# Performance work log

Hardware: AMD Instinct MI355X
Metric: run time of the kernel (lower is better)

## Reference

```python
import jax, jax.numpy as jnp
import numpy as np

B, N, E, D, R, T, L = 4, 20000, 320000, 64, 64, 1000, 6
LN_EPS = 1e-5


def setup_inputs() -> dict:
    key = jax.random.key(0)
    ks = jax.random.split(key, 20)
    inp = {
        "edge_index": jax.random.randint(ks[0], (2, E), 0, N),
        "edge_type": jax.random.randint(ks[1], (E,), 0, R),
        "relation_representations": jax.random.normal(ks[2], (B, R, D), jnp.float32),
        "h_index": jax.random.randint(ks[3], (B,), 0, N),
        "r_index": jax.random.randint(ks[4], (B,), 0, R),
        "t_index": jax.random.randint(ks[5], (B, T), 0, N),
        "edge_weight": jnp.ones((E,), jnp.float32),
        # per-layer relation-projection MLP (Linear,ReLU,Linear)
        "rp_w1": jax.random.normal(ks[6], (L, D, D), jnp.float32) / np.sqrt(D),
        "rp_b1": jnp.zeros((L, D), jnp.float32),
        "rp_w2": jax.random.normal(ks[7], (L, D, D), jnp.float32) / np.sqrt(D),
        "rp_b2": jnp.zeros((L, D), jnp.float32),
        # per-layer update linear: concat([input, aggregated]) -> D
        "conv_w": jax.random.normal(ks[8], (L, 2 * D, D), jnp.float32) / np.sqrt(2 * D),
        "conv_b": jnp.zeros((L, D), jnp.float32),
        "ln_g": jnp.ones((L, D), jnp.float32),
        "ln_b": jnp.zeros((L, D), jnp.float32),
        # final MLP (num_mlp_layers=2): feature_dim = D (last hidden) + D (query) = 2D
        "mlp_w1": jax.random.normal(ks[9], (2 * D, 2 * D), jnp.float32) / np.sqrt(2 * D),
        "mlp_b1": jnp.zeros((2 * D,), jnp.float32),
        "mlp_w2": jax.random.normal(ks[10], (2 * D, 1), jnp.float32) / np.sqrt(2 * D),
        "mlp_b2": jnp.zeros((1,), jnp.float32),
    }
    return inp


def reference(edge_index, edge_type, relation_representations, h_index, r_index,
              t_index, edge_weight, rp_w1, rp_b1, rp_w2, rp_b2, conv_w, conv_b,
              ln_g, ln_b, mlp_w1, mlp_b1, mlp_w2, mlp_b2):
    # --- boundary: scatter query embedding onto source node per query ---
    query = relation_representations[jnp.arange(B), r_index]              # [B, D]
    boundary = jnp.zeros((B, N, D), jnp.float32).at[jnp.arange(B), h_index].add(query)
    src, dst = edge_index[0], edge_index[1]

    def layer(x, params):
        w1, b1, w2, b2, cw, cb, g, b = params
        # project_relations MLP on query relation representations
        rel = jax.nn.relu(jnp.einsum('brd,de->bre', relation_representations, w1) + b1)
        rel = jnp.einsum('brd,de->bre', rel, w2) + b2                     # [B, R, D]
        # distmult message: h[src] * rel[edge_type], weighted
        msg = x[:, src, :] * rel[:, edge_type, :] * edge_weight[None, :, None]  # [B, E, D]
        agg = jax.ops.segment_sum(msg.transpose(1, 0, 2), dst,
                                  num_segments=N).transpose(1, 0, 2)
        agg = agg + boundary                                              # boundary self-loop
        h = jnp.concatenate([x, agg], axis=-1) @ cw + cb                  # [B, N, D]
        mu = h.mean(-1, keepdims=True)
        var = h.var(-1, keepdims=True)
        h = (h - mu) * jax.lax.rsqrt(var + LN_EPS) * g + b                # layer norm
        h = jax.nn.relu(h)
        return h + x, None                                                # short_cut

    x, _ = jax.lax.scan(layer, boundary,
                        (rp_w1, rp_b1, rp_w2, rp_b2, conv_w, conv_b, ln_g, ln_b))
    node_query = jnp.broadcast_to(query[:, None, :], (B, N, D))
    output = jnp.concatenate([x, node_query], axis=-1)                    # [B, N, 2D]
    feat = jnp.take_along_axis(output, t_index[:, :, None], axis=1)       # [B, T, 2D]
    h = jax.nn.relu(feat @ mlp_w1 + mlp_b1)
    score = (h @ mlp_w2 + mlp_b2).squeeze(-1)                             # [B, T]
    return score
```

## Files before the change

kernel.cpp:

```cpp
#include <hip/hip_runtime.h>
#include <hip/hip_fp16.h>

#define NB 4
#define NN 20000
#define NE 320000
#define ND 64
#define NR 64
#define NT 1000
#define NL 6
#define LN_EPS 1e-5f
#define CAP 64

typedef _Float16 half8 __attribute__((ext_vector_type(8)));
typedef _Float16 half4v __attribute__((ext_vector_type(4)));
typedef float floatx4 __attribute__((ext_vector_type(4)));


__global__ void __launch_bounds__(256)
prep1(int* __restrict__ cnt,
      const float* __restrict__ cw, _Float16* __restrict__ cwt,
      const float* __restrict__ relrep, const int* __restrict__ r_index,
      float* __restrict__ query,
      const float* __restrict__ rp_w1, const float* __restrict__ rp_b1,
      const float* __restrict__ rp_w2, const float* __restrict__ rp_b2,
      __half* __restrict__ rel16) {
    int blk = blockIdx.x, tid = threadIdx.x;
    if (blk < 79) {
        int i = blk * 256 + tid;
        if (i < NN) cnt[i] = 0;
    } else if (blk < 271) {
        int i = (blk - 79) * 256 + tid;
        int l = i >> 13, rem = i & 8191, k = rem >> 6, n = rem & 63;
        cwt[l * 8192 + n * 128 + k] = (_Float16)cw[i];
    } else if (blk == 271) {
        int b = tid >> 6, d = tid & 63;
        query[tid] = relrep[(b * NR + r_index[b]) * ND + d];
    } else {
        int u = blk - 272;
        int l = u >> 6, r = u & 63;
        int b = tid >> 6, j = tid & 63;
        const float* w1 = rp_w1 + l * ND * ND;
        const float* w2 = rp_w2 + l * ND * ND;
        float xin = relrep[(b * NR + r) * ND + j];
        float acc = rp_b1[l * ND + j];
        #pragma unroll 8
        for (int k = 0; k < ND; ++k) acc += __shfl(xin, k) * w1[k * ND + j];
        float hmid = fmaxf(acc, 0.f);
        float outv = rp_b2[l * ND + j];
        #pragma unroll 8
        for (int k = 0; k < ND; ++k) outv += __shfl(hmid, k) * w2[k * ND + j];
        rel16[l * (NR * NB * ND) + (r * NB + b) * ND + j] = __float2half(outv);
    }
}

__global__ void __launch_bounds__(256)
prep2(const int* __restrict__ ei, const int* __restrict__ et,
      const float* __restrict__ ew, int* __restrict__ cnt,
      int4* __restrict__ epack) {
    int e = blockIdx.x * 256 + threadIdx.x;
    int d = ei[NE + e];
    int p = atomicAdd(&cnt[d], 1);
    if (p < CAP)
        epack[d * CAP + p] = make_int4(ei[e], et[e], __float_as_int(ew[e]), 0);
}

__device__ __forceinline__ float2 h2f(unsigned u) {
    __half2 h = *(__half2*)&u;
    return __half22float2(h);
}
__device__ __forceinline__ __half2 u2h2(unsigned u) { return *(__half2*)&u; }

__device__ __forceinline__ void conv_ln_epilogue(
        _Float16* A16, float* sD, int wv, int lane, int n,
        const _Float16* __restrict__ cwt, const float* __restrict__ cb,
        const float* __restrict__ g, const float* __restrict__ bb,
        __half* __restrict__ xo16) {
    __syncthreads();
    {
        int m = lane & 15, quad = lane >> 4;
        int ncol = wv * 16 + m;
        floatx4 acc = {0.f, 0.f, 0.f, 0.f};
        #pragma unroll
        for (int k0 = 0; k0 < 128; k0 += 32) {
            half8 a = *(const half8*)&A16[m * 136 + k0 + quad * 8];
            half8 bfr = *(const half8*)&cwt[ncol * 128 + k0 + quad * 8];
            acc = __builtin_amdgcn_mfma_f32_16x16x32_f16(a, bfr, acc, 0, 0, 0);
        }
        #pragma unroll
        for (int rg = 0; rg < 4; ++rg)
            sD[(quad * 4 + rg) * 65 + ncol] = acc[rg];
    }
    __syncthreads();
    float gl = g[lane], bl = bb[lane], cbl = cb[lane];
    #pragma unroll
    for (int b = 0; b < NB; ++b) {
        float acc = sD[(wv * 4 + b) * 65 + lane] + cbl;
        float s = acc, s2 = acc * acc;
        #pragma unroll
        for (int o = 32; o > 0; o >>= 1) { s += __shfl_xor(s, o); s2 += __shfl_xor(s2, o); }
        float mu  = s * (1.f / ND);
        float var = s2 * (1.f / ND) - mu * mu;
        float hn  = (acc - mu) * rsqrtf(var + LN_EPS) * gl + bl;
        float xvf = (float)A16[(wv * 4 + b) * 136 + lane];
        float v   = fmaxf(hn, 0.f) + xvf;
        xo16[(n * NB + b) * ND + lane] = __float2half(v);
    }
}

__global__ void __launch_bounds__(256)
fused_layer_first(const __half* __restrict__ rel16,
                  const int* __restrict__ cnt, const int4* __restrict__ epack,
                  const float* __restrict__ query, const int* __restrict__ h_index,
                  const _Float16* __restrict__ cwt, const float* __restrict__ cb,
                  const float* __restrict__ g, const float* __restrict__ bb,
                  __half* __restrict__ xo16) {
    __shared__ _Float16 A16[16 * 136];
    __shared__ float sD[16 * 65];
    int wv = threadIdx.x >> 6;
    int lane = threadIdx.x & 63;
    int n = blockIdx.x * 4 + wv;
    int cn = min(cnt[n], CAP);
    int bidx = lane >> 4, c4 = (lane & 15) << 2;
    int hb = h_index[bidx];

    const uint2* __restrict__ r2 = (const uint2*)rel16;
    float4 q4 = ((const float4*)query)[lane];
    half4v qh;
    qh.x = (_Float16)q4.x; qh.y = (_Float16)q4.y;
    qh.z = (_Float16)q4.z; qh.w = (_Float16)q4.w;
    float qx = (float)qh.x, qy = (float)qh.y, qz = (float)qh.z, qw = (float)qh.w;

    float4 agg4 = make_float4(0.f, 0.f, 0.f, 0.f);
    {
        int4 ed = make_int4(0, 0, 0, 0);
        if (lane < cn) ed = epack[n * CAP + lane];
        for (int j = 0; j < cn; ++j) {
            int s   = __shfl(ed.x, j);
            int t   = __shfl(ed.y, j);
            float w = __int_as_float(__shfl(ed.z, j));
            if (s == hb) {
                uint2 ra = r2[t * 64 + lane];
                float2 q0 = h2f(ra.x), q1 = h2f(ra.y);
                agg4.x = fmaf(qx * q0.x, w, agg4.x);
                agg4.y = fmaf(qy * q0.y, w, agg4.y);
                agg4.z = fmaf(qz * q1.x, w, agg4.z);
                agg4.w = fmaf(qw * q1.y, w, agg4.w);
            }
        }
    }
    if (n == hb) {
        agg4.x += q4.x; agg4.y += q4.y; agg4.z += q4.z; agg4.w += q4.w;
    }
    {
        int r = wv * 4 + bidx;
        half4v xh = {0, 0, 0, 0};
        if (n == hb) xh = qh;
        *(half4v*)&A16[r * 136 + c4] = xh;
        half4v ah;
        ah.x = (_Float16)agg4.x; ah.y = (_Float16)agg4.y;
        ah.z = (_Float16)agg4.z; ah.w = (_Float16)agg4.w;
        *(half4v*)&A16[r * 136 + 64 + c4] = ah;
    }
    conv_ln_epilogue(A16, sD, wv, lane, n, cwt, cb, g, bb, xo16);
}

__global__ void __launch_bounds__(256)
fused_layer(const __half* __restrict__ x16, const __half* __restrict__ rel16,
            const int* __restrict__ cnt, const int4* __restrict__ epack,
            const float* __restrict__ query, const int* __restrict__ h_index,
            const _Float16* __restrict__ cwt, const float* __restrict__ cb,
            const float* __restrict__ g, const float* __restrict__ bb,
            __half* __restrict__ xo16) {
    __shared__ _Float16 A16[16 * 136];
    __shared__ float sD[16 * 65];
    int wv = threadIdx.x >> 6;
    int lane = threadIdx.x & 63;
    int n = blockIdx.x * 4 + wv;
    int cn = min(cnt[n], CAP);
    int hf = lane >> 5, sub = lane & 31;

    const uint4* __restrict__ x4 = (const uint4*)x16;
    const uint4* __restrict__ r4 = (const uint4*)rel16;

    float acc[8] = {0.f, 0.f, 0.f, 0.f, 0.f, 0.f, 0.f, 0.f};
    {
        int4 ed = make_int4(0, 0, 0, 0);
        if (lane < cn) ed = epack[n * CAP + lane];
        int j = 0;
        for (; j + 4 <= cn; j += 4) {
            int ja = j + hf, jb = j + 2 + hf;
            int sa = __shfl(ed.x, ja), ta = __shfl(ed.y, ja);
            int sb = __shfl(ed.x, jb), tb = __shfl(ed.y, jb);
            float wa = __int_as_float(__shfl(ed.z, ja));
            float wb = __int_as_float(__shfl(ed.z, jb));
            uint4 xa = x4[sa * 32 + sub], ra = r4[ta * 32 + sub];
            uint4 xb = x4[sb * 32 + sub], rb = r4[tb * 32 + sub];
            __half2 p0, p1, p2, p3;
            p0 = __hmul2(u2h2(xa.x), u2h2(ra.x));
            p1 = __hmul2(u2h2(xa.y), u2h2(ra.y));
            p2 = __hmul2(u2h2(xa.z), u2h2(ra.z));
            p3 = __hmul2(u2h2(xa.w), u2h2(ra.w));
            acc[0] = fmaf(__low2float(p0),  wa, acc[0]);
            acc[1] = fmaf(__high2float(p0), wa, acc[1]);
            acc[2] = fmaf(__low2float(p1),  wa, acc[2]);
            acc[3] = fmaf(__high2float(p1), wa, acc[3]);
            acc[4] = fmaf(__low2float(p2),  wa, acc[4]);
            acc[5] = fmaf(__high2float(p2), wa, acc[5]);
            acc[6] = fmaf(__low2float(p3),  wa, acc[6]);
            acc[7] = fmaf(__high2float(p3), wa, acc[7]);
            p0 = __hmul2(u2h2(xb.x), u2h2(rb.x));
            p1 = __hmul2(u2h2(xb.y), u2h2(rb.y));
            p2 = __hmul2(u2h2(xb.z), u2h2(rb.z));
            p3 = __hmul2(u2h2(xb.w), u2h2(rb.w));
            acc[0] = fmaf(__low2float(p0),  wb, acc[0]);
            acc[1] = fmaf(__high2float(p0), wb, acc[1]);
            acc[2] = fmaf(__low2float(p1),  wb, acc[2]);
            acc[3] = fmaf(__high2float(p1), wb, acc[3]);
            acc[4] = fmaf(__low2float(p2),  wb, acc[4]);
            acc[5] = fmaf(__high2float(p2), wb, acc[5]);
            acc[6] = fmaf(__low2float(p3),  wb, acc[6]);
            acc[7] = fmaf(__high2float(p3), wb, acc[7]);
        }
        for (; j < cn; j += 2) {
            int ja = j + hf;
            int sa = __shfl(ed.x, ja), ta = __shfl(ed.y, ja);
            float wa = __int_as_float(__shfl(ed.z, ja));
            uint4 xa = x4[sa * 32 + sub], ra = r4[ta * 32 + sub];
            __half2 p0 = __hmul2(u2h2(xa.x), u2h2(ra.x));
            __half2 p1 = __hmul2(u2h2(xa.y), u2h2(ra.y));
            __half2 p2 = __hmul2(u2h2(xa.z), u2h2(ra.z));
            __half2 p3 = __hmul2(u2h2(xa.w), u2h2(ra.w));
            acc[0] = fmaf(__low2float(p0),  wa, acc[0]);
            acc[1] = fmaf(__high2float(p0), wa, acc[1]);
            acc[2] = fmaf(__low2float(p1),  wa, acc[2]);
            acc[3] = fmaf(__high2float(p1), wa, acc[3]);
            acc[4] = fmaf(__low2float(p2),  wa, acc[4]);
            acc[5] = fmaf(__high2float(p2), wa, acc[5]);
            acc[6] = fmaf(__low2float(p3),  wa, acc[6]);
            acc[7] = fmaf(__high2float(p3), wa, acc[7]);
        }
    }
    #pragma unroll
    for (int k = 0; k < 8; ++k) acc[k] += __shfl_xor(acc[k], 32);
    int bq = sub >> 3, ch = (sub & 7) << 3;
    if (hf == 0) {
        if (n == h_index[bq]) {
            const float* qp = query + bq * 64 + ch;
            #pragma unroll
            for (int k = 0; k < 8; ++k) acc[k] += qp[k];
        }
        int r = wv * 4 + bq;
        half8 ah;
        #pragma unroll
        for (int k = 0; k < 8; ++k) ah[k] = (_Float16)acc[k];
        *(half8*)&A16[r * 136 + 64 + ch] = ah;
    }
    {
        int bidx = lane >> 4, c4 = (lane & 15) << 2;
        int r = wv * 4 + bidx;
        const uint2* __restrict__ x2 = (const uint2*)x16;
        uint2 xraw = x2[(n * NB + bidx) * 16 + (lane & 15)];
        *(uint2*)&A16[r * 136 + c4] = xraw;
    }
    conv_ln_epilogue(A16, sD, wv, lane, n, cwt, cb, g, bb, xo16);
}

__global__ void final_score(const __half* __restrict__ x16, const float* __restrict__ query,
                            const int* __restrict__ t_index,
                            const float* __restrict__ w1, const float* __restrict__ b1,
                            const float* __restrict__ w2, const float* __restrict__ b2,
                            float* __restrict__ out) {
    int gid = blockIdx.x * 4 + (threadIdx.x >> 6);
    int lane = threadIdx.x & 63;
    int b = gid / NT;
    int ti = t_index[gid];
    float xv = __half2float(x16[(ti * NB + b) * ND + lane]);
    float qv = query[b * ND + lane];
    float a0 = b1[lane], a1 = b1[lane + 64];
    #pragma unroll 8
    for (int k = 0; k < ND; ++k) {
        float f = __shfl(xv, k);
        a0 += f * w1[k * 128 + lane];
        a1 += f * w1[k * 128 + lane + 64];
    }
    #pragma unroll 8
    for (int k = 0; k < ND; ++k) {
        float f = __shfl(qv, k);
        a0 += f * w1[(ND + k) * 128 + lane];
        a1 += f * w1[(ND + k) * 128 + lane + 64];
    }
    a0 = fmaxf(a0, 0.f);
    a1 = fmaxf(a1, 0.f);
    float p = a0 * w2[lane] + a1 * w2[lane + 64];
    #pragma unroll
    for (int o = 32; o > 0; o >>= 1) p += __shfl_xor(p, o);
    if (lane == 0) out[gid] = p + b2[0];
}

extern "C" void kernel_launch(void* const* d_in, const int* in_sizes, int n_in,
                              void* d_out, int out_size, void* d_ws, size_t ws_size,
                              hipStream_t stream) {
    const int*   edge_index  = (const int*)d_in[0];
    const int*   edge_type   = (const int*)d_in[1];
    const float* relrep      = (const float*)d_in[2];
    const int*   h_index     = (const int*)d_in[3];
    const int*   r_index     = (const int*)d_in[4];
    const int*   t_index     = (const int*)d_in[5];
    const float* edge_weight = (const float*)d_in[6];
    const float* rp_w1  = (const float*)d_in[7];
    const float* rp_b1  = (const float*)d_in[8];
    const float* rp_w2  = (const float*)d_in[9];
    const float* rp_b2  = (const float*)d_in[10];
    const float* conv_w = (const float*)d_in[11];
    const float* conv_b = (const float*)d_in[12];
    const float* ln_g   = (const float*)d_in[13];
    const float* ln_b   = (const float*)d_in[14];
    const float* mlp_w1 = (const float*)d_in[15];
    const float* mlp_b1 = (const float*)d_in[16];
    const float* mlp_w2 = (const float*)d_in[17];
    const float* mlp_b2 = (const float*)d_in[18];
    float* out = (float*)d_out;

    const int BND = NB * NN * ND;
    const int RELSZ = NR * NB * ND;
    float*    ws     = (float*)d_ws;
    float*    query  = ws;
    __half*   rel16  = (__half*)(query + 256);
    __half*   x16a   = rel16 + NL * RELSZ;
    __half*   x16b   = x16a + BND;
    _Float16* cwt16  = (_Float16*)(x16b + BND);
    int4*     epack  = (int4*)(cwt16 + NL * 8192);
    int*      cnt    = (int*)(epack + NN * CAP);

    prep1<<<656, 256, 0, stream>>>(cnt, conv_w, cwt16, relrep, r_index, query,
                                   rp_w1, rp_b1, rp_w2, rp_b2, rel16);
    prep2<<<NE / 256, 256, 0, stream>>>(edge_index, edge_type, edge_weight,
                                        cnt, epack);

    __half* mc = x16a; __half* mn = x16b;
    fused_layer_first<<<NN / 4, 256, 0, stream>>>(rel16, cnt, epack,
                                                  query, h_index,
                                                  cwt16, conv_b, ln_g, ln_b, mc);
    for (int l = 1; l < NL; ++l) {
        fused_layer<<<NN / 4, 256, 0, stream>>>(mc, rel16 + l * RELSZ, cnt, epack,
                                                query, h_index,
                                                cwt16 + l * 8192, conv_b + l * ND,
                                                ln_g + l * ND, ln_b + l * ND, mn);
        __half* th = mc; mc = mn; mn = th;
    }
    final_score<<<NB * NT / 4, 256, 0, stream>>>(mc, query, t_index,
                                                 mlp_w1, mlp_b1, mlp_w2, mlp_b2, out);
}
```

Before: 325.7 us.

## Fuse all message-passing layers and scoring into one cooperative persistent kernel

Replaces the seven per-layer kernel launches (first layer, five layers, final score) with one cooperative kernel of 1024 blocks. The blocks loop over node groups and use grid-wide syncs between layers. This removes launch gaps and tail effects between layers, at the cost of grid barriers and fixed occupancy (4 blocks per CU requested via launch bounds). If the cooperative launch fails, it falls back to the original multi-launch path.

```diff
diff --git a/kernel.cpp b/kernel.cpp
--- a/kernel.cpp
+++ b/kernel.cpp
@@ -1,5 +1,6 @@
 #include <hip/hip_runtime.h>
 #include <hip/hip_fp16.h>
+#include <hip/hip_cooperative_groups.h>
 
 #define NB 4
 #define NN 20000
@@ -10,6 +11,7 @@
 #define NL 6
 #define LN_EPS 1e-5f
 #define CAP 64
+#define GRID 1024
 
 typedef _Float16 half8 __attribute__((ext_vector_type(8)));
 typedef _Float16 half4v __attribute__((ext_vector_type(4)));
@@ -107,18 +109,14 @@
     }
 }
 
-__global__ void __launch_bounds__(256)
-fused_layer_first(const __half* __restrict__ rel16,
-                  const int* __restrict__ cnt, const int4* __restrict__ epack,
-                  const float* __restrict__ query, const int* __restrict__ h_index,
-                  const _Float16* __restrict__ cwt, const float* __restrict__ cb,
-                  const float* __restrict__ g, const float* __restrict__ bb,
-                  __half* __restrict__ xo16) {
-    __shared__ _Float16 A16[16 * 136];
-    __shared__ float sD[16 * 65];
-    int wv = threadIdx.x >> 6;
-    int lane = threadIdx.x & 63;
-    int n = blockIdx.x * 4 + wv;
+__device__ __forceinline__ void first_unit(
+        int n, int wv, int lane,
+        const __half* __restrict__ rel16, const int* __restrict__ cnt,
+        const int4* __restrict__ epack, const float* __restrict__ query,
+        const int* __restrict__ h_index, const _Float16* __restrict__ cwt,
+        const float* __restrict__ cb, const float* __restrict__ g,
+        const float* __restrict__ bb, __half* __restrict__ xo16,
+        _Float16* A16, float* sD) {
     int cn = min(cnt[n], CAP);
     int bidx = lane >> 4, c4 = (lane & 15) << 2;
     int hb = h_index[bidx];
@@ -164,18 +162,14 @@
     conv_ln_epilogue(A16, sD, wv, lane, n, cwt, cb, g, bb, xo16);
 }
 
-__global__ void __launch_bounds__(256)
-fused_layer(const __half* __restrict__ x16, const __half* __restrict__ rel16,
-            const int* __restrict__ cnt, const int4* __restrict__ epack,
-            const float* __restrict__ query, const int* __restrict__ h_index,
-            const _Float16* __restrict__ cwt, const float* __restrict__ cb,
-            const float* __restrict__ g, const float* __restrict__ bb,
-            __half* __restrict__ xo16) {
-    __shared__ _Float16 A16[16 * 136];
-    __shared__ float sD[16 * 65];
-    int wv = threadIdx.x >> 6;
-    int lane = threadIdx.x & 63;
-    int n = blockIdx.x * 4 + wv;
+__device__ __forceinline__ void layer_unit(
+        int n, int wv, int lane,
+        const __half* __restrict__ x16, const __half* __restrict__ rel16,
+        const int* __restrict__ cnt, const int4* __restrict__ epack,
+        const float* __restrict__ query, const int* __restrict__ h_index,
+        const _Float16* __restrict__ cwt, const float* __restrict__ cb,
+        const float* __restrict__ g, const float* __restrict__ bb,
+        __half* __restrict__ xo16, _Float16* A16, float* sD) {
     int cn = min(cnt[n], CAP);
     int hf = lane >> 5, sub = lane & 31;
 
@@ -265,13 +259,12 @@
     conv_ln_epilogue(A16, sD, wv, lane, n, cwt, cb, g, bb, xo16);
 }
 
-__global__ void final_score(const __half* __restrict__ x16, const float* __restrict__ query,
-                            const int* __restrict__ t_index,
-                            const float* __restrict__ w1, const float* __restrict__ b1,
-                            const float* __restrict__ w2, const float* __restrict__ b2,
-                            float* __restrict__ out) {
-    int gid = blockIdx.x * 4 + (threadIdx.x >> 6);
-    int lane = threadIdx.x & 63;
+__device__ __forceinline__ void score_unit(
+        int gid, int lane, const __half* __restrict__ x16,
+        const float* __restrict__ query, const int* __restrict__ t_index,
+        const float* __restrict__ w1, const float* __restrict__ b1,
+        const float* __restrict__ w2, const float* __restrict__ b2,
+        float* __restrict__ out) {
     int b = gid / NT;
     int ti = t_index[gid];
     float xv = __half2float(x16[(ti * NB + b) * ND + lane]);
@@ -295,6 +288,84 @@
     #pragma unroll
     for (int o = 32; o > 0; o >>= 1) p += __shfl_xor(p, o);
     if (lane == 0) out[gid] = p + b2[0];
+}
+
+__global__ void __launch_bounds__(256)
+fused_layer_first_k(const __half* __restrict__ rel16,
+                    const int* __restrict__ cnt, const int4* __restrict__ epack,
+                    const float* __restrict__ query, const int* __restrict__ h_index,
+                    const _Float16* __restrict__ cwt, const float* __restrict__ cb,
+                    const float* __restrict__ g, const float* __restrict__ bb,
+                    __half* __restrict__ xo16) {
+    __shared__ _Float16 A16[16 * 136];
+    __shared__ float sD[16 * 65];
+    int wv = threadIdx.x >> 6, lane = threadIdx.x & 63;
+    first_unit(blockIdx.x * 4 + wv, wv, lane, rel16, cnt, epack, query,
+               h_index, cwt, cb, g, bb, xo16, A16, sD);
+}
+
+__global__ void __launch_bounds__(256)
+fused_layer_k(const __half* __restrict__ x16, const __half* __restrict__ rel16,
+              const int* __restrict__ cnt, const int4* __restrict__ epack,
+              const float* __restrict__ query, const int* __restrict__ h_index,
+              const _Float16* __restrict__ cwt, const float* __restrict__ cb,
+              const float* __restrict__ g, const float* __restrict__ bb,
+              __half* __restrict__ xo16) {
+    __shared__ _Float16 A16[16 * 136];
+    __shared__ float sD[16 * 65];
+    int wv = threadIdx.x >> 6, lane = threadIdx.x & 63;
+    layer_unit(blockIdx.x * 4 + wv, wv, lane, x16, rel16, cnt, epack, query,
+               h_index, cwt, cb, g, bb, xo16, A16, sD);
+}
+
+__global__ void __launch_bounds__(256)
+final_score_k(const __half* __restrict__ x16, const float* __restrict__ query,
+              const int* __restrict__ t_index,
+              const float* __restrict__ w1, const float* __restrict__ b1,
+              const float* __restrict__ w2, const float* __restrict__ b2,
+              float* __restrict__ out) {
+    int wv = threadIdx.x >> 6, lane = threadIdx.x & 63;
+    score_unit(blockIdx.x * 4 + wv, lane, x16, query, t_index, w1, b1, w2, b2, out);
+}
+
+__global__ void __launch_bounds__(256, 4)
+mega(__half* xa, __half* xb, const int* cnt, const int4* epack,
+     const __half* rel16, const float* query, const int* h_index,
+     const _Float16* cwt, const float* conv_b, const float* ln_g,
+     const float* ln_b, const int* t_index, const float* mw1,
+     const float* mb1, const float* mw2, const float* mb2, float* out) {
+    cooperative_groups::grid_group grid = cooperative_groups::this_grid();
+    __shared__ _Float16 A16[16 * 136];
+    __shared__ float sD[16 * 65];
+    int wv = threadIdx.x >> 6;
+    int lane = threadIdx.x & 63;
+
+    for (int u = blockIdx.x; u < NN / 4; u += GRID) {
+        __syncthreads();
+        first_unit(u * 4 + wv, wv, lane, rel16, cnt, epack, query, h_index,
+                   cwt, conv_b, ln_g, ln_b, xa, A16, sD);
+    }
+    grid.sync();
+    __half* cur = xa;
+    __half* nxt = xb;
+    for (int l = 1; l < NL; ++l) {
+        const __half*    r_l  = rel16 + l * (NR * NB * ND);
+        const _Float16*  w_l  = cwt + l * 8192;
+        const float*     cb_l = conv_b + l * ND;
+        const float*     g_l  = ln_g + l * ND;
+        const float*     b_l  = ln_b + l * ND;
+        for (int u = blockIdx.x; u < NN / 4; u += GRID) {
+            __syncthreads();
+            layer_unit(u * 4 + wv, wv, lane, cur, r_l, cnt, epack, query,
+                       h_index, w_l, cb_l, g_l, b_l, nxt, A16, sD);
+        }
+        grid.sync();
+        __half* t = cur; cur = nxt; nxt = t;
+    }
+    for (int u = blockIdx.x; u < (NB * NT) / 4; u += GRID) {
+        score_unit(u * 4 + wv, lane, cur, query, t_index,
+                   mw1, mb1, mw2, mb2, out);
+    }
 }
 
 extern "C" void kernel_launch(void* const* d_in, const int* in_sizes, int n_in,
@@ -337,17 +408,45 @@
     prep2<<<NE / 256, 256, 0, stream>>>(edge_index, edge_type, edge_weight,
                                         cnt, epack);
 
-    __half* mc = x16a; __half* mn = x16b;
-    fused_layer_first<<<NN / 4, 256, 0, stream>>>(rel16, cnt, epack,
-                                                  query, h_index,
-                                                  cwt16, conv_b, ln_g, ln_b, mc);
-    for (int l = 1; l < NL; ++l) {
-        fused_layer<<<NN / 4, 256, 0, stream>>>(mc, rel16 + l * RELSZ, cnt, epack,
-                                                query, h_index,
-                                                cwt16 + l * 8192, conv_b + l * ND,
-                                                ln_g + l * ND, ln_b + l * ND, mn);
-        __half* th = mc; mc = mn; mn = th;
-    }
-    final_score<<<NB * NT / 4, 256, 0, stream>>>(mc, query, t_index,
-                                                 mlp_w1, mlp_b1, mlp_w2, mlp_b2, out);
-}
+    __half*          a_xa  = x16a;
+    __half*          a_xb  = x16b;
+    const int*       a_cnt = cnt;
+    const int4*      a_ep  = epack;
+    const __half*    a_rel = rel16;
+    const float*     a_q   = query;
+    const int*       a_h   = h_index;
+    const _Float16*  a_cw  = cwt16;
+    const float*     a_cb  = conv_b;
+    const float*     a_g   = ln_g;
+    const float*     a_b   = ln_b;
+    const int*       a_t   = t_index;
+    const float*     a_w1  = mlp_w1;
+    const float*     a_b1  = mlp_b1;
+    const float*     a_w2  = mlp_w2;
+    const float*     a_b2  = mlp_b2;
+    float*           a_out = out;
+    void* args[17] = {&a_xa, &a_xb, &a_cnt, &a_ep, &a_rel, &a_q, &a_h,
+                      &a_cw, &a_cb, &a_g, &a_b, &a_t, &a_w1, &a_b1,
+                      &a_w2, &a_b2, &a_out};
+    hipError_t cerr = hipLaunchCooperativeKernel((void*)mega, dim3(GRID),
+                                                 dim3(256), args, 0, stream);
+    if (cerr != hipSuccess) {
+        (void)hipGetLastError();
+        __half* mc = x16a; __half* mn = x16b;
+        fused_layer_first_k<<<NN / 4, 256, 0, stream>>>(rel16, cnt, epack,
+                                                        query, h_index, cwt16,
+                                                        conv_b, ln_g, ln_b, mc);
+        for (int l = 1; l < NL; ++l) {
+            fused_layer_k<<<NN / 4, 256, 0, stream>>>(mc, rel16 + l * RELSZ,
+                                                      cnt, epack, query, h_index,
+                                                      cwt16 + l * 8192,
+                                                      conv_b + l * ND,
+                                                      ln_g + l * ND,
+                                                      ln_b + l * ND, mn);
+            __half* th = mc; mc = mn; mn = th;
+        }
+        final_score_k<<<NB * NT / 4, 256, 0, stream>>>(mc, query, t_index,
+                                                       mlp_w1, mlp_b1,
+                                                       mlp_w2, mlp_b2, out);
+    }
+}
```

New measurement: 1.160 ms. +256.1%, slower.
